# Kernel optimization log

Hardware: AMD Instinct MI355X
Metric: run time of the kernel (lower is better)

The kernel has to match this reference:

```python
import jax, jax.numpy as jnp
import numpy as np

N_NODES = 50000
N_EDGES = 600000
IN_F = 256
OUT_F = 128


def setup_inputs() -> dict:
    key = jax.random.key(0)
    k1, k2, k3, k4, k5, k6 = jax.random.split(key, 6)
    x = jax.random.normal(k1, (N_NODES, IN_F), dtype=jnp.float32)
    edge_rows = jax.random.randint(k2, (N_EDGES,), 0, N_NODES, dtype=jnp.int32)
    edge_cols = jax.random.randint(k3, (N_EDGES,), 0, N_NODES, dtype=jnp.int32)
    edge_vals = jax.random.uniform(k4, (N_EDGES,), dtype=jnp.float32)
    # xavier_uniform init bound for weight [in, out]
    bound = float(np.sqrt(6.0 / (IN_F + OUT_F)))
    weight = jax.random.uniform(k5, (IN_F, OUT_F), dtype=jnp.float32, minval=-bound, maxval=bound)
    bias = jax.random.normal(k6, (OUT_F,), dtype=jnp.float32) * 0.02
    return {"x": x, "edge_rows": edge_rows, "edge_cols": edge_cols,
            "edge_vals": edge_vals, "weight": weight, "bias": bias}


def reference(x, edge_rows, edge_cols, edge_vals, weight, bias):
    # support = x @ W            [N, out]
    support = x @ weight
    # sparse adj @ support: out[r] += val * support[c] for each edge (r, c, val)
    msgs = edge_vals[:, None] * support[edge_cols]           # [E, out]
    agg = jax.ops.segment_sum(msgs, edge_rows, num_segments=N_NODES)  # [N, out]
    return agg + bias
```

## Files before the change

### kernel.cpp

```cpp
#include <hip/hip_runtime.h>
#include <hip/hip_bf16.h>

#define N_NODES 50000
#define N_EDGES 600000
#define IN_F 256
#define OUT_F 128
#define GEMM_BLOCKS 196
#define NBUCK 391
#define NBUCKA 392
#define BROWS 128
#define NBLK_E 256
#define EPB 2344
#define ITERS 5
#define CAP 2048

typedef __bf16 bf16x8 __attribute__((ext_vector_type(8)));
typedef __bf16 bf16x2 __attribute__((ext_vector_type(2)));
typedef float  f32x4  __attribute__((ext_vector_type(4)));

__device__ __forceinline__ void async_copy16(void* lds, const void* g) {
    __builtin_amdgcn_global_load_lds(
        (const __attribute__((address_space(1))) void*)g,
        (__attribute__((address_space(3))) void*)lds, 16, 0, 0);
}

__global__ __launch_bounds__(256) void gcn_prep(const float* __restrict__ w,
                                                __bf16* __restrict__ wt_sw,
                                                int* __restrict__ cursor) {
    if (blockIdx.x == 128) {
        for (int j = threadIdx.x; j < NBUCKA; j += 256) cursor[j] = 0;
        return;
    }
    int i = blockIdx.x * 256 + threadIdx.x;
    int n = i >> 8;
    int k = (i & 255) ^ ((n & 7) << 3);
    wt_sw[i] = (__bf16)w[k * OUT_F + n];
}

#define GLOAD(P, ks)                                    \
    P##_0 = *(const float4*)(xp0 + (ks) * 32);          \
    P##_1 = *(const float4*)(xp0 + (ks) * 32 + 4);      \
    P##_2 = *(const float4*)(xp1 + (ks) * 32);          \
    P##_3 = *(const float4*)(xp1 + (ks) * 32 + 4);

#define KSTEP(P, ks) {                                                             \
    bf16x8 af0 = { (__bf16)P##_0.x, (__bf16)P##_0.y, (__bf16)P##_0.z, (__bf16)P##_0.w, \
                   (__bf16)P##_1.x, (__bf16)P##_1.y, (__bf16)P##_1.z, (__bf16)P##_1.w };\
    bf16x8 af1 = { (__bf16)P##_2.x, (__bf16)P##_2.y, (__bf16)P##_2.z, (__bf16)P##_2.w, \
                   (__bf16)P##_3.x, (__bf16)P##_3.y, (__bf16)P##_3.z, (__bf16)P##_3.w };\
    _Pragma("unroll")                                                              \
    for (int nt = 0; nt < 8; nt++) {                                               \
        int nrow = nt * 16 + m;                                                    \
        const bf16x8 bf = *(const bf16x8*)(smem + (nrow << 9) +                    \
                            (((ks) * 64 + quad * 16) ^ ((nrow & 7) << 4)));        \
        acc0[nt] = __builtin_amdgcn_mfma_f32_16x16x32_bf16(af0, bf, acc0[nt], 0, 0, 0); \
        acc1[nt] = __builtin_amdgcn_mfma_f32_16x16x32_bf16(af1, bf, acc1[nt], 0, 0, 0); \
    } }

__global__ __launch_bounds__(512, 3) void gcn_gemm_scatter(const float* __restrict__ x,
                                                           const __bf16* __restrict__ wt_sw,
                                                           __bf16* __restrict__ support,
                                                           const int* __restrict__ erows,
                                                           const int* __restrict__ ecols,
                                                           const float* __restrict__ evals,
                                                           int* __restrict__ cursor,
                                                           int2* __restrict__ bucketed) {
    __shared__ char smem[65536];
    const int t = threadIdx.x;

    if (blockIdx.x >= GEMM_BLOCKS) {
        int b = blockIdx.x - GEMM_BLOCKS;
        int* lh = (int*)smem;
        for (int j = t; j < NBUCKA; j += 512) lh[j] = 0;
        __syncthreads();
        int e0 = b * EPB;
        int e1 = e0 + EPB; if (e1 > N_EDGES) e1 = N_EDGES;
        int myr[ITERS];
#pragma unroll
        for (int j = 0; j < ITERS; j++) {
            int e = e0 + j * 512 + t;
            myr[j] = -1;
            if (e < e1) {
                int r = erows[e];
                myr[j] = r;
                atomicAdd(&lh[r >> 7], 1);
            }
        }
        __syncthreads();
        if (t < NBUCKA) {
            int c = lh[t];
            lh[t] = c ? atomicAdd(&cursor[t], c) : 0;
        }
        __syncthreads();
#pragma unroll
        for (int j = 0; j < ITERS; j++) {
            int r = myr[j];
            if (r >= 0) {
                int e = e0 + j * 512 + t;
                int g = r >> 7;
                int rank = atomicAdd(&lh[g], 1);
                if (rank < CAP)
                    bucketed[((size_t)g << 11) + rank] =
                        make_int2(((r & 127) << 16) | ecols[e],
                                  __float_as_int(evals[e]));
            }
        }
        return;
    }

    const int wave = t >> 6;
    const int lane = t & 63;
    const int m    = lane & 15;
    const int quad = lane >> 4;

    {
        const char* gW = (const char*)wt_sw + wave * 1024 + lane * 16;
        char* lW = smem + wave * 1024;
#pragma unroll
        for (int it = 0; it < 8; it++)
            async_copy16(lW + it * 8192, gW + it * 8192);
    }
    __syncthreads();

    const int row0 = blockIdx.x * 256 + wave * 32;
    int r0 = row0 + m;
    int r1 = row0 + 16 + m;
    const float* xp0 = x + (size_t)(r0 < N_NODES ? r0 : 0) * IN_F + quad * 8;
    const float* xp1 = x + (size_t)(r1 < N_NODES ? r1 : 0) * IN_F + quad * 8;

    f32x4 acc0[8], acc1[8];
#pragma unroll
    for (int nt = 0; nt < 8; nt++) {
        acc0[nt] = (f32x4){0.f, 0.f, 0.f, 0.f};
        acc1[nt] = (f32x4){0.f, 0.f, 0.f, 0.f};
    }

    float4 A_0, A_1, A_2, A_3, B_0, B_1, B_2, B_3, C_0, C_1, C_2, C_3;
    GLOAD(A, 0) GLOAD(B, 1)
    GLOAD(C, 2) KSTEP(A, 0)
    GLOAD(A, 3) KSTEP(B, 1)
    GLOAD(B, 4) KSTEP(C, 2)
    GLOAD(C, 5) KSTEP(A, 3)
    GLOAD(A, 6) KSTEP(B, 4)
    GLOAD(B, 7) KSTEP(C, 5)
    KSTEP(A, 6)
    KSTEP(B, 7)

    __syncthreads();
#pragma unroll
    for (int nt = 0; nt < 8; nt++) {
        int cb = (nt * 16 + m) * 2;
#pragma unroll
        for (int r = 0; r < 4; r++) {
            int lr0 = wave * 32 + quad * 4 + r;
            int lr1 = lr0 + 16;
            *(__bf16*)(smem + (lr0 << 8) + (cb ^ ((lr0 & 7) << 4))) = (__bf16)acc0[nt][r];
            *(__bf16*)(smem + (lr1 << 8) + (cb ^ ((lr1 & 7) << 4))) = (__bf16)acc1[nt][r];
        }
    }
    __syncthreads();
    {
        int row  = t >> 1;
        int half = t & 1;
        int g = blockIdx.x * 256 + row;
        if (g < N_NODES) {
            char* dst = (char*)(support + (size_t)g * OUT_F) + half * 128;
#pragma unroll
            for (int j = 0; j < 8; j++) {
                int boff = (half * 128 + j * 16) ^ ((row & 7) << 4);
                *(bf16x8*)(dst + j * 16) = *(const bf16x8*)(smem + (row << 8) + boff);
            }
        }
    }
}

__global__ __launch_bounds__(512, 8) void gcn_agg_sorted(const __bf16* __restrict__ support,
                                                         const int2* __restrict__ bucketed,
                                                         const int* __restrict__ cursor,
                                                         const float* __restrict__ bias,
                                                         float* __restrict__ out) {
    __shared__ int2 se_raw[CAP];
    __shared__ int2 se[CAP];
    __shared__ int  lh[BROWS];
    __shared__ int  rs[BROWS];
    __shared__ int  run[BROWS];
    __shared__ int  sc[512];
    const int g  = blockIdx.x;
    const int t  = threadIdx.x;
    const int wv = t >> 6, ln = t & 63;

    const int beg = g << 11;
    int ne = cursor[g]; if (ne > CAP) ne = CAP; if (ne < 0) ne = 0;

    if (t < BROWS) lh[t] = 0;
    __syncthreads();
    for (int i = t; i < ne; i += 512) {
        int2 cv = bucketed[beg + i];
        se_raw[i] = cv;
        atomicAdd(&lh[cv.x >> 16], 1);
    }
    __syncthreads();

    int v = (t < BROWS) ? lh[t] : 0;
    sc[t] = v;
    __syncthreads();
#pragma unroll
    for (int off = 1; off < BROWS; off <<= 1) {
        int x = (t >= off) ? sc[t - off] : 0;
        __syncthreads();
        sc[t] += x;
        __syncthreads();
    }
    if (t < BROWS) { rs[t] = sc[t] - v; run[t] = sc[t] - v; }
    __syncthreads();

    for (int i = t; i < ne; i += 512) {
        int2 cv = se_raw[i];
        int p = atomicAdd(&run[cv.x >> 16], 1);
        se[p] = make_int2(cv.x & 0xFFFF, cv.y);
    }
    __syncthreads();

    const int grow0 = g * BROWS;
    const __bf16* spL = support + ln * 2;
    const float2 bias2 = *(const float2*)&bias[ln * 2];
    for (int rr = 0; rr < 16; rr++) {
        int row  = wv * 16 + rr;
        int grow = grow0 + row;
        if (grow >= N_NODES) break;
        float2 acc = bias2;
        int b0 = rs[row];
        int b1 = b0 + lh[row];
        int j = b0;
        for (; j + 3 < b1; j += 4) {
            int2 e0 = se[j];
            int2 e1 = se[j + 1];
            int2 e2 = se[j + 2];
            int2 e3 = se[j + 3];
            bf16x2 s0 = *(const bf16x2*)(spL + (size_t)e0.x * OUT_F);
            bf16x2 s1 = *(const bf16x2*)(spL + (size_t)e1.x * OUT_F);
            bf16x2 s2 = *(const bf16x2*)(spL + (size_t)e2.x * OUT_F);
            bf16x2 s3 = *(const bf16x2*)(spL + (size_t)e3.x * OUT_F);
            float v0 = __int_as_float(e0.y);
            float v1 = __int_as_float(e1.y);
            float v2 = __int_as_float(e2.y);
            float v3 = __int_as_float(e3.y);
            acc.x += v0 * (float)s0.x + v1 * (float)s1.x;
            acc.y += v0 * (float)s0.y + v1 * (float)s1.y;
            acc.x += v2 * (float)s2.x + v3 * (float)s3.x;
            acc.y += v2 * (float)s2.y + v3 * (float)s3.y;
        }
        for (; j < b1; j++) {
            int2 e0 = se[j];
            bf16x2 s0 = *(const bf16x2*)(spL + (size_t)e0.x * OUT_F);
            float v0 = __int_as_float(e0.y);
            acc.x += v0 * (float)s0.x;
            acc.y += v0 * (float)s0.y;
        }
        *(float2*)&out[(size_t)grow * OUT_F + ln * 2] = acc;
    }
}

static inline size_t align_up(size_t v, size_t a) { return (v + a - 1) & ~(a - 1); }

extern "C" void kernel_launch(void* const* d_in, const int* in_sizes, int n_in,
                              void* d_out, int out_size, void* d_ws, size_t ws_size,
                              hipStream_t stream) {
    const float* x     = (const float*)d_in[0];
    const int*   erows = (const int*)d_in[1];
    const int*   ecols = (const int*)d_in[2];
    const float* evals = (const float*)d_in[3];
    const float* w     = (const float*)d_in[4];
    const float* bias  = (const float*)d_in[5];
    float* out = (float*)d_out;

    size_t off = 0;
    __bf16* support   = (__bf16*)((char*)d_ws + off);
    off = align_up(off + (size_t)N_NODES * OUT_F * 2, 64);
    __bf16* wt_sw     = (__bf16*)((char*)d_ws + off);
    off = align_up(off + (size_t)IN_F * OUT_F * 2, 64);
    int*    cursor    = (int*)((char*)d_ws + off);
    off = align_up(off + (size_t)NBUCKA * 4, 64);
    int2*   bucketed  = (int2*)((char*)d_ws + off);

    gcn_prep<<<129, 256, 0, stream>>>(w, wt_sw, cursor);

    gcn_gemm_scatter<<<GEMM_BLOCKS + NBLK_E, 512, 0, stream>>>(
        x, wt_sw, support, erows, ecols, evals, cursor, bucketed);

    gcn_agg_sorted<<<NBUCK, 512, 0, stream>>>(support, bucketed, cursor, bias, out);
}
```

Baseline: 162.3 us.

## Halve aggregation bucket size to 64 rows and unroll gather loop by eight

Bucket rows in groups of 64 instead of 128, doubling the number of aggregation blocks (782) and halving per-block LDS staging (CAP 1024), so more blocks spread across CUs and occupancy rises. Each wave now handles 8 rows instead of 16. The gather loop is unrolled to 8 edges with two independent accumulators to expose more memory-level parallelism. Risks: CAP 1024 overflow is unlikely for 64 rows at about 12 edges per row, but more cursor atomics and more block setup overhead.

```diff
diff --git a/kernel.cpp b/kernel.cpp
--- a/kernel.cpp
+++ b/kernel.cpp
@@ -6,13 +6,13 @@
 #define IN_F 256
 #define OUT_F 128
 #define GEMM_BLOCKS 196
-#define NBUCK 391
-#define NBUCKA 392
-#define BROWS 128
+#define NBUCK 782
+#define NBUCKA 784
+#define BROWS 64
 #define NBLK_E 256
 #define EPB 2344
 #define ITERS 5
-#define CAP 2048
+#define CAP 1024
 
 typedef __bf16 bf16x8 __attribute__((ext_vector_type(8)));
 typedef __bf16 bf16x2 __attribute__((ext_vector_type(2)));
@@ -83,13 +83,13 @@
             if (e < e1) {
                 int r = erows[e];
                 myr[j] = r;
-                atomicAdd(&lh[r >> 7], 1);
+                atomicAdd(&lh[r >> 6], 1);
             }
         }
         __syncthreads();
-        if (t < NBUCKA) {
-            int c = lh[t];
-            lh[t] = c ? atomicAdd(&cursor[t], c) : 0;
+        for (int j0 = t; j0 < NBUCKA; j0 += 512) {
+            int c = lh[j0];
+            lh[j0] = c ? atomicAdd(&cursor[j0], c) : 0;
         }
         __syncthreads();
 #pragma unroll
@@ -97,11 +97,11 @@
             int r = myr[j];
             if (r >= 0) {
                 int e = e0 + j * 512 + t;
-                int g = r >> 7;
+                int g = r >> 6;
                 int rank = atomicAdd(&lh[g], 1);
                 if (rank < CAP)
-                    bucketed[((size_t)g << 11) + rank] =
-                        make_int2(((r & 127) << 16) | ecols[e],
+                    bucketed[((size_t)g << 10) + rank] =
+                        make_int2(((r & 63) << 16) | ecols[e],
                                   __float_as_int(evals[e]));
             }
         }
@@ -184,12 +184,12 @@
     __shared__ int  lh[BROWS];
     __shared__ int  rs[BROWS];
     __shared__ int  run[BROWS];
-    __shared__ int  sc[512];
+    __shared__ int  sc[128];
     const int g  = blockIdx.x;
     const int t  = threadIdx.x;
     const int wv = t >> 6, ln = t & 63;
 
-    const int beg = g << 11;
+    const int beg = g << 10;
     int ne = cursor[g]; if (ne > CAP) ne = CAP; if (ne < 0) ne = 0;
 
     if (t < BROWS) lh[t] = 0;
@@ -201,17 +201,24 @@
     }
     __syncthreads();
 
-    int v = (t < BROWS) ? lh[t] : 0;
-    sc[t] = v;
+    if (t < 128) {
+        int v = (t < BROWS) ? lh[t] : 0;
+        sc[t] = v;
+    }
     __syncthreads();
 #pragma unroll
     for (int off = 1; off < BROWS; off <<= 1) {
-        int x = (t >= off) ? sc[t - off] : 0;
-        __syncthreads();
-        sc[t] += x;
-        __syncthreads();
-    }
-    if (t < BROWS) { rs[t] = sc[t] - v; run[t] = sc[t] - v; }
+        int x = 0;
+        if (t < 128 && t >= off) x = sc[t - off];
+        __syncthreads();
+        if (t < 128) sc[t] += x;
+        __syncthreads();
+    }
+    if (t < BROWS) {
+        int v = lh[t];
+        rs[t] = sc[t] - v;
+        run[t] = sc[t] - v;
+    }
     __syncthreads();
 
     for (int i = t; i < ne; i += 512) {
@@ -224,14 +231,49 @@
     const int grow0 = g * BROWS;
     const __bf16* spL = support + ln * 2;
     const float2 bias2 = *(const float2*)&bias[ln * 2];
-    for (int rr = 0; rr < 16; rr++) {
-        int row  = wv * 16 + rr;
+    for (int rr = 0; rr < 8; rr++) {
+        int row  = wv * 8 + rr;
         int grow = grow0 + row;
         if (grow >= N_NODES) break;
         float2 acc = bias2;
+        float2 accB = make_float2(0.f, 0.f);
         int b0 = rs[row];
         int b1 = b0 + lh[row];
         int j = b0;
+        for (; j + 7 < b1; j += 8) {
+            int2 e0 = se[j];
+            int2 e1 = se[j + 1];
+            int2 e2 = se[j + 2];
+            int2 e3 = se[j + 3];
+            int2 e4 = se[j + 4];
+            int2 e5 = se[j + 5];
+            int2 e6 = se[j + 6];
+            int2 e7 = se[j + 7];
+            bf16x2 s0 = *(const bf16x2*)(spL + (size_t)e0.x * OUT_F);
+            bf16x2 s1 = *(const bf16x2*)(spL + (size_t)e1.x * OUT_F);
+            bf16x2 s2 = *(const bf16x2*)(spL + (size_t)e2.x * OUT_F);
+            bf16x2 s3 = *(const bf16x2*)(spL + (size_t)e3.x * OUT_F);
+            bf16x2 s4 = *(const bf16x2*)(spL + (size_t)e4.x * OUT_F);
+            bf16x2 s5 = *(const bf16x2*)(spL + (size_t)e5.x * OUT_F);
+            bf16x2 s6 = *(const bf16x2*)(spL + (size_t)e6.x * OUT_F);
+            bf16x2 s7 = *(const bf16x2*)(spL + (size_t)e7.x * OUT_F);
+            float v0 = __int_as_float(e0.y);
+            float v1 = __int_as_float(e1.y);
+            float v2 = __int_as_float(e2.y);
+            float v3 = __int_as_float(e3.y);
+            float v4 = __int_as_float(e4.y);
+            float v5 = __int_as_float(e5.y);
+            float v6 = __int_as_float(e6.y);
+            float v7 = __int_as_float(e7.y);
+            acc.x  += v0 * (float)s0.x + v1 * (float)s1.x;
+            acc.y  += v0 * (float)s0.y + v1 * (float)s1.y;
+            accB.x += v2 * (float)s2.x + v3 * (float)s3.x;
+            accB.y += v2 * (float)s2.y + v3 * (float)s3.y;
+            acc.x  += v4 * (float)s4.x + v5 * (float)s5.x;
+            acc.y  += v4 * (float)s4.y + v5 * (float)s5.y;
+            accB.x += v6 * (float)s6.x + v7 * (float)s7.x;
+            accB.y += v6 * (float)s6.y + v7 * (float)s7.y;
+        }
         for (; j + 3 < b1; j += 4) {
             int2 e0 = se[j];
             int2 e1 = se[j + 1];
@@ -245,10 +287,10 @@
             float v1 = __int_as_float(e1.y);
             float v2 = __int_as_float(e2.y);
             float v3 = __int_as_float(e3.y);
-            acc.x += v0 * (float)s0.x + v1 * (float)s1.x;
-            acc.y += v0 * (float)s0.y + v1 * (float)s1.y;
-            acc.x += v2 * (float)s2.x + v3 * (float)s3.x;
-            acc.y += v2 * (float)s2.y + v3 * (float)s3.y;
+            acc.x  += v0 * (float)s0.x + v1 * (float)s1.x;
+            acc.y  += v0 * (float)s0.y + v1 * (float)s1.y;
+            accB.x += v2 * (float)s2.x + v3 * (float)s3.x;
+            accB.y += v2 * (float)s2.y + v3 * (float)s3.y;
         }
         for (; j < b1; j++) {
             int2 e0 = se[j];
@@ -257,6 +299,8 @@
             acc.x += v0 * (float)s0.x;
             acc.y += v0 * (float)s0.y;
         }
+        acc.x += accB.x;
+        acc.y += accB.y;
         *(float2*)&out[(size_t)grow * OUT_F + ln * 2] = acc;
     }
 }
```

New measurement: 149.2 us. 8.1% less time.
